# Performance work log

Measured on AMD Instinct MI355X. Metric: run time of the kernel, lower is better.

The kernel has to match this reference:

```python
import jax, jax.numpy as jnp
import numpy as np

BN_EPS = 1e-5

def _conv(x, w, b, pad):
    # x: [B,C,H,W], w: [O,I,kh,kw] -> [B,O,H,W]
    y = jax.lax.conv_general_dilated(x, w, window_strides=(1, 1),
                                     padding=[(pad, pad), (pad, pad)],
                                     dimension_numbers=("NCHW", "OIHW", "NCHW"))
    return y + b[None, :, None, None]

def setup_inputs() -> dict:
    key = jax.random.key(0)
    ks = jax.random.split(key, 5)
    B, Cin, H, W = 2, 256, 80, 80
    Ck, Cv, Cout = 128, 256, 256
    std = 0.02  # matches torch normal_(0, 0.02) init
    return {
        "x": jax.random.normal(ks[0], (B, Cin, H, W), jnp.float32),
        "wk": std * jax.random.normal(ks[1], (Ck, Cin, 1, 1), jnp.float32),
        "bk": jnp.zeros((Ck,), jnp.float32),
        "gamma": jnp.ones((Ck,), jnp.float32),
        "beta": jnp.zeros((Ck,), jnp.float32),
        "rmean": jnp.zeros((Ck,), jnp.float32),
        "rvar": jnp.ones((Ck,), jnp.float32),
        "wv": std * jax.random.normal(ks[2], (Cv, Cin, 3, 3), jnp.float32),
        "bv": jnp.zeros((Cv,), jnp.float32),
        "ww": std * jax.random.normal(ks[3], (Cout, Cv, 1, 1), jnp.float32),
        "bw": jnp.zeros((Cout,), jnp.float32),
    }

def reference(x, wk, bk, gamma, beta, rmean, rvar, wv, bv, ww, bw):
    B, Cin, H, W = x.shape
    Ck, Cv = wk.shape[0], wv.shape[0]
    N = H * W

    # f_key == f_query (shared module): 1x1 conv + BatchNorm (inference stats)
    kq = _conv(x, wk, bk, pad=0)                      # [B,Ck,H,W]
    inv = gamma / jnp.sqrt(rvar + BN_EPS)
    kq = kq * inv[None, :, None, None] + (beta - rmean * inv)[None, :, None, None]
    kq = kq.reshape(B, Ck, N)                          # key layout [B,Ck,N]

    # f_value: 3x3 conv
    value = _conv(x, wv, bv, pad=1).reshape(B, Cv, N)  # [B,Cv,N]

    # sim_map = query^T @ key -> [B,N,N], full softmax over last dim
    sim = jnp.einsum("bcn,bcm->bnm", kq, kq)
    sim = jax.nn.softmax(sim, axis=-1)

    # context = sim @ value^T -> [B,N,Cv] -> [B,Cv,H,W]
    ctx = jnp.einsum("bnm,bcm->bcn", sim, value).reshape(B, Cv, H, W)

    out = _conv(ctx, ww, bw, pad=0) + x                # residual
    return out
```

## Files before the change

### kernel.cpp

```cpp
#include <hip/hip_runtime.h>
#include <math.h>

#define NB   2
#define CIN  256
#define IMH  80
#define IMW  80
#define NPIX (IMH*IMW)
#define CK   128
#define CVC  256
#define COUTC 256
#define BN_EPS 1e-5f
#define HP   82
#define WP   82
#define NMC  (NPIX / 64)
#define LOG2E 1.4426950408889634f
#define M0L  28.853900817779268f

typedef short sx8 __attribute__((ext_vector_type(8)));
typedef short sx4 __attribute__((ext_vector_type(4)));
typedef float f32x4 __attribute__((ext_vector_type(4)));

__device__ __forceinline__ short f2bf(float f) {
    unsigned u = __builtin_bit_cast(unsigned, f);
    u += 0x7fffu + ((u >> 16) & 1u);
    return (short)(u >> 16);
}
__device__ __forceinline__ float bf2f(short s) {
    unsigned u = ((unsigned)(unsigned short)s) << 16;
    return __builtin_bit_cast(float, u);
}
__device__ __forceinline__ int pk_bf16(float a, float b) {
    unsigned ua = __builtin_bit_cast(unsigned, a) + 0x8000u;
    unsigned ub = __builtin_bit_cast(unsigned, b) + 0x8000u;
    return __builtin_amdgcn_perm(ub, ua, 0x07060302);
}

#define WVT_BLKS 256
#define WWB_BLKS 256
#define WKB_BLKS 128
__global__ __launch_bounds__(256) void prep_kernel(
    const float* __restrict__ wv, const float* __restrict__ ww,
    const float* __restrict__ wk, const float* __restrict__ bk,
    const float* __restrict__ gamma, const float* __restrict__ beta,
    const float* __restrict__ rmean, const float* __restrict__ rvar,
    short* __restrict__ wvt, short* __restrict__ wwb,
    short* __restrict__ wkb, float* __restrict__ bias2)
{
    __shared__ short L[9][258];
    const int tid = threadIdx.x;
    const int bx  = blockIdx.x;

    if (bx < WVT_BLKS) {
        const float* src = wv + (size_t)bx * 2304;
        #pragma unroll
        for (int i = 0; i < 9; ++i) {
            int m = i * 256 + tid;
            L[m % 9][m / 9] = f2bf(src[m]);
        }
        __syncthreads();
        #pragma unroll
        for (int j = 0; j < 9; ++j)
            wvt[(size_t)j * (CVC * CIN) + bx * 256 + tid] = L[j][tid];
    } else if (bx < WVT_BLKS + WWB_BLKS) {
        int idx = (bx - WVT_BLKS) * 256 + tid;
        wwb[idx] = f2bf(ww[idx]);
    } else {
        int idx = (bx - WVT_BLKS - WWB_BLKS) * 256 + tid;
        int ck = idx >> 8;
        float inv = gamma[ck] * rsqrtf(rvar[ck] + BN_EPS);
        wkb[idx] = f2bf(wk[idx] * inv);
        if (idx < CK) {
            float invi = gamma[idx] * rsqrtf(rvar[idx] + BN_EPS);
            bias2[idx] = (bk[idx] - rmean[idx]) * invi + beta[idx];
        }
    }
}

__global__ __launch_bounds__(256) void padkq_kernel(
    const float* __restrict__ x, const short* __restrict__ wkb,
    const float* __restrict__ bias2, short* __restrict__ xpad,
    short* __restrict__ kqT)
{
    __shared__ short T[64][258];
    const int tid = threadIdx.x;
    const int n0  = blockIdx.x * 64;
    const int b   = blockIdx.y;
    const float* xb = x + (size_t)b * CIN * NPIX;

    #pragma unroll 4
    for (int i = 0; i < 64; ++i) {
        int e = tid + i * 256;
        int pix = e & 63, c = e >> 6;
        T[pix][c] = f2bf(xb[(size_t)c * NPIX + n0 + pix]);
    }
    __syncthreads();

    #pragma unroll
    for (int i = 0; i < 8; ++i) {
        int e   = tid + i * 256;
        int pix = e >> 5;
        int cp  = (e & 31) * 8;
        int np  = n0 + pix;
        int hp  = np / IMW + 1, wp = np % IMW + 1;
        sx8 v = *(const sx8*)&T[pix][cp];
        *(sx8*)&xpad[(((size_t)b * HP + hp) * WP + wp) * CIN + cp] = v;
    }

    {
        int e = blockIdx.x * 256 + tid;
        if (e < 324 * 32) {
            int p = e >> 5, c8 = (e & 31) * 8;
            int hp, wp;
            if      (p < 82)  { hp = 0;       wp = p;       }
            else if (p < 164) { hp = 81;      wp = p - 82;  }
            else if (p < 244) { hp = p - 163; wp = 0;       }
            else              { hp = p - 243; wp = 81;      }
            sx8 z = {};
            *(sx8*)&xpad[(((size_t)b * HP + hp) * WP + wp) * CIN + c8] = z;
        }
    }

    const int wid  = tid >> 6;
    const int lane = tid & 63;
    const int l15  = lane & 15;
    const int quad = lane >> 4;
    const int ck0  = wid * 32;

    f32x4 acc[2][4];
    #pragma unroll
    for (int at = 0; at < 2; ++at)
        #pragma unroll
        for (int nt = 0; nt < 4; ++nt)
            acc[at][nt] = (f32x4){0.f, 0.f, 0.f, 0.f};

    for (int kc = 0; kc < CIN / 32; ++kc) {
        sx8 af0 = *(const sx8*)&wkb[(size_t)(ck0 + l15) * CIN + kc * 32 + quad * 8];
        sx8 af1 = *(const sx8*)&wkb[(size_t)(ck0 + 16 + l15) * CIN + kc * 32 + quad * 8];
        #pragma unroll
        for (int nt = 0; nt < 4; ++nt) {
            sx8 bf = *(const sx8*)&T[nt * 16 + l15][kc * 32 + quad * 8];
            acc[0][nt] = __builtin_amdgcn_mfma_f32_16x16x32_bf16(af0, bf, acc[0][nt], 0, 0, 0);
            acc[1][nt] = __builtin_amdgcn_mfma_f32_16x16x32_bf16(af1, bf, acc[1][nt], 0, 0, 0);
        }
    }

    __syncthreads();

    #pragma unroll
    for (int at = 0; at < 2; ++at) {
        f32x4 b4 = *(const f32x4*)&bias2[ck0 + at * 16 + quad * 4];
        #pragma unroll
        for (int nt = 0; nt < 4; ++nt)
            #pragma unroll
            for (int r = 0; r < 4; ++r)
                T[nt * 16 + l15][ck0 + at * 16 + quad * 4 + r] = f2bf(acc[at][nt][r] + b4[r]);
    }
    __syncthreads();
    #pragma unroll
    for (int it = 0; it < 4; ++it) {
        int e = tid + it * 256;
        int row = e >> 4, c8 = (e & 15) * 8;
        *(sx8*)&kqT[((size_t)b * NPIX + n0 + row) * CK + c8] = *(const sx8*)&T[row][c8];
    }
}

#define CSTRIDE 36
__global__ __launch_bounds__(512) void conv3_kernel(
    const short* __restrict__ xpad, const short* __restrict__ wvt,
    const float* __restrict__ bv, short* __restrict__ valF)
{
    __shared__ __align__(16) short Xs[2][6 * 18 * CSTRIDE];

    const int tid  = threadIdx.x;
    const int wid  = tid >> 6;
    const int lane = tid & 63;
    const int l15  = lane & 15;
    const int quad = lane >> 4;

    const int rowT = blockIdx.x / 5, colT = blockIdx.x % 5;
    const int h0 = rowT * 4, w0 = colT * 16;
    const int cv0 = blockIdx.y * 128 + wid * 16;
    const int b   = blockIdx.z;

    const short* xb = xpad + (size_t)b * HP * WP * CIN;

    const int rc  = tid >> 2, l4 = tid & 3;
    const int row = rc / 18, col = rc % 18;
    const bool sv = (tid < 432);
    const short* sptr = &xb[(((size_t)(h0 + row)) * WP + (w0 + col)) * CIN + l4 * 8];
    const int sdst = rc * CSTRIDE + l4 * 8;

    f32x4 acc[4];
    #pragma unroll
    for (int r = 0; r < 4; ++r) acc[r] = (f32x4){0.f, 0.f, 0.f, 0.f};

    sx8 v = {};
    if (sv) {
        v = *(const sx8*)&sptr[0];
        *(sx8*)&Xs[0][sdst] = v;
    }
    __syncthreads();

    for (int cc = 0; cc < CIN / 32; ++cc) {
        const int cur = cc & 1;
        if (cc + 1 < CIN / 32 && sv)
            v = *(const sx8*)&sptr[(cc + 1) * 32];

        #pragma unroll
        for (int dw = 0; dw < 3; ++dw) {
            sx8 Bf[6];
            #pragma unroll
            for (int rr = 0; rr < 6; ++rr)
                Bf[rr] = *(const sx8*)&Xs[cur][(rr * 18 + l15 + dw) * CSTRIDE + quad * 8];
            #pragma unroll
            for (int dh = 0; dh < 3; ++dh) {
                int tap = dh * 3 + dw;
                sx8 Af = *(const sx8*)&wvt[((size_t)(tap * 256 + cv0 + l15)) * CIN + cc * 32 + quad * 8];
                #pragma unroll
                for (int r = 0; r < 4; ++r)
                    acc[r] = __builtin_amdgcn_mfma_f32_16x16x32_bf16(Af, Bf[r + dh], acc[r], 0, 0, 0);
            }
        }

        if (cc + 1 < CIN / 32 && sv)
            *(sx8*)&Xs[cur ^ 1][sdst] = v;
        __syncthreads();
    }

    f32x4 bvv = *(const f32x4*)&bv[cv0 + quad * 4];
    const int cvt = cv0 >> 4;
    #pragma unroll
    for (int r = 0; r < 4; ++r) {
        int n  = (h0 + r) * IMW + w0 + l15;
        int mc = n >> 6, s2 = (n >> 5) & 1, qm = (n >> 3) & 3, mi = n & 7;
        size_t base = ((((size_t)(b * NMC + mc) * 16 + cvt) * 2 + s2) * 4 + qm) * 128;
        #pragma unroll
        for (int reg = 0; reg < 4; ++reg)
            valF[base + (quad * 4 + reg) * 8 + mi] = f2bf(acc[r][reg] + bvv[reg]);
    }
}

#define TQ 64
#define TK 64
#define KS_LD 132
#define PS_LD 72

template<int SP>
__global__ __launch_bounds__(512) void attn_kernel(
    const short* __restrict__ kqT, const short* __restrict__ valF,
    short* __restrict__ opart, float* __restrict__ lpart)
{
    constexpr int NCc  = NPIX / SP / 64;
    constexpr int SPSH = (SP == 4) ? 3 : 2;

    __shared__ __align__(16) short Ks[TK][KS_LD];
    __shared__ __align__(16) short Pb[TQ][PS_LD];
    __shared__ float lqs[2][64];

    const int tid  = threadIdx.x;
    const int wid  = tid >> 6;
    const int lane = tid & 63;
    const int l15  = lane & 15;
    const int quad = lane >> 4;
    const int qw   = wid & 3;
    const int mh   = wid >> 2;

    const int blk = blockIdx.x;
    const int b   = blk & 1;
    const int sp  = (blk >> 1) & (SP - 1);
    const int n0  = (blk >> SPSH) * TQ;
    const int mb  = sp * (NPIX / SP);

    const short* kqb = kqT + (size_t)b * NPIX * CK;
    const short* vbase = valF + ((size_t)(b * NMC + sp * NCc) * 16 + wid * 2) * 1024
                              + (size_t)lane * 8;

    const int srow = tid >> 4;
    const int sc8  = (tid & 15) * 8;

    sx8 qf[4];
    #pragma unroll
    for (int s = 0; s < 4; ++s)
        qf[s] = *(const sx8*)&kqb[(size_t)(n0 + qw * 16 + l15) * CK + s * 32 + quad * 8];

    sx8 kreg[2];
    #pragma unroll
    for (int p = 0; p < 2; ++p)
        kreg[p] = *(const sx8*)&kqb[(size_t)(mb + srow + p * 32) * CK + sc8];
    #pragma unroll
    for (int p = 0; p < 2; ++p)
        *(sx8*)&Ks[srow + p * 32][sc8] = kreg[p];

    sx8 vreg[4];
    #pragma unroll
    for (int ct = 0; ct < 2; ++ct)
        #pragma unroll
        for (int s2 = 0; s2 < 2; ++s2)
            vreg[ct * 2 + s2] = *(const sx8*)&vbase[ct * 1024 + s2 * 512];

    float lq = 0.f;
    f32x4 acc[4][2];
    #pragma unroll
    for (int qt = 0; qt < 4; ++qt)
        #pragma unroll
        for (int ct = 0; ct < 2; ++ct)
            acc[qt][ct] = (f32x4){0.f, 0.f, 0.f, 0.f};

    __syncthreads();

    for (int i = 0; i < NCc; ++i) {
        if (i + 1 < NCc) {
            #pragma unroll
            for (int p = 0; p < 2; ++p)
                kreg[p] = *(const sx8*)&kqb[(size_t)(mb + (i + 1) * TK + srow + p * 32) * CK + sc8];
        }

        f32x4 st[2];
        #pragma unroll
        for (int t2 = 0; t2 < 2; ++t2) st[t2] = (f32x4){0.f, 0.f, 0.f, 0.f};
        #pragma unroll
        for (int s = 0; s < 4; ++s) {
            sx8 af[2];
            #pragma unroll
            for (int t2 = 0; t2 < 2; ++t2)
                af[t2] = *(const sx8*)&Ks[mh * 32 + t2 * 16 + l15][s * 32 + quad * 8];
            #pragma unroll
            for (int t2 = 0; t2 < 2; ++t2)
                st[t2] = __builtin_amdgcn_mfma_f32_16x16x32_bf16(af[t2], qf[s], st[t2], 0, 0, 0);
        }

        __syncthreads();

        #pragma unroll
        for (int t2 = 0; t2 < 2; ++t2)
            #pragma unroll
            for (int r = 0; r < 4; ++r)
                st[t2][r] = exp2f(fmaf(st[t2][r], LOG2E, -M0L));

        if (i + 1 < NCc) {
            #pragma unroll
            for (int p = 0; p < 2; ++p)
                *(sx8*)&Ks[srow + p * 32][sc8] = kreg[p];
        }

        #pragma unroll
        for (int t2 = 0; t2 < 2; ++t2) {
            int2 pw;
            pw.x = pk_bf16(st[t2][0], st[t2][1]);
            pw.y = pk_bf16(st[t2][2], st[t2][3]);
            *(int2*)&Pb[qw * 16 + l15][mh * 32 + t2 * 16 + quad * 4] = pw;
        }

        lq += (st[0][0] + st[0][1]) + (st[0][2] + st[0][3])
            + (st[1][0] + st[1][1]) + (st[1][2] + st[1][3]);

        __syncthreads();

        #pragma unroll
        for (int s2 = 0; s2 < 2; ++s2) {
            sx8 pa[4];
            #pragma unroll
            for (int qt = 0; qt < 4; ++qt)
                pa[qt] = *(const sx8*)&Pb[qt * 16 + l15][s2 * 32 + quad * 8];
            #pragma unroll
            for (int ct = 0; ct < 2; ++ct) {
                #pragma unroll
                for (int qt = 0; qt < 4; ++qt)
                    acc[qt][ct] = __builtin_amdgcn_mfma_f32_16x16x32_bf16(pa[qt], vreg[ct * 2 + s2], acc[qt][ct], 0, 0, 0);
            }
        }

        if (i + 1 < NCc) {
            #pragma unroll
            for (int ct = 0; ct < 2; ++ct)
                #pragma unroll
                for (int s2 = 0; s2 < 2; ++s2)
                    vreg[ct * 2 + s2] = *(const sx8*)&vbase[(size_t)(i + 1) * 16384 + ct * 1024 + s2 * 512];
        }
    }

    lq += __shfl_xor(lq, 16);
    lq += __shfl_xor(lq, 32);
    if (quad == 0)
        lqs[mh][qw * 16 + l15] = lq;

    size_t obase = (size_t)(sp * NB + b) * NPIX + n0;
    #pragma unroll
    for (int qt = 0; qt < 4; ++qt)
        #pragma unroll
        for (int ct = 0; ct < 2; ++ct) {
            int cv = wid * 32 + ct * 16 + l15;
            #pragma unroll
            for (int r = 0; r < 4; ++r)
                opart[(obase + qt * 16 + quad * 4 + r) * CVC + cv] = f2bf(acc[qt][ct][r]);
        }

    __syncthreads();
    if (tid < 64)
        lpart[obase + tid] = lqs[0][tid] + lqs[1][tid];
}

#define BS_LD 40
template<int SP>
__global__ __launch_bounds__(512) void out_kernel(
    const short* __restrict__ opart, const float* __restrict__ lpart,
    const short* __restrict__ wwb, const float* __restrict__ bw,
    const float* __restrict__ x, float* __restrict__ out)
{
    __shared__ __align__(16) short Bs[2][64][BS_LD];
    __shared__ float rinvs[64];

    const int tid  = threadIdx.x;
    const int wid  = tid >> 6;
    const int lane = tid & 63;
    const int l15  = lane & 15;
    const int quad = lane >> 4;

    const int n0  = blockIdx.x * 64;
    const int co0 = blockIdx.y * 128 + wid * 16;
    const int b   = blockIdx.z;

    if (tid < 64) {
        int n = n0 + tid;
        float ls = 0.f;
        #pragma unroll
        for (int s = 0; s < SP; ++s)
            ls += lpart[(size_t)(s * NB + b) * NPIX + n];
        rinvs[tid] = 1.f / ls;
    }

    const int srow = tid >> 2;
    const int sc8  = (tid & 3) * 8;
    const short* op0 = opart + ((size_t)b * NPIX + n0 + srow) * CVC + sc8;
    constexpr size_t SSTR = (size_t)NB * NPIX * CVC;
    const bool sv = (tid < 256);

    __syncthreads();

    if (sv) {
        float ri = rinvs[srow];
        float sacc[8] = {0.f, 0.f, 0.f, 0.f, 0.f, 0.f, 0.f, 0.f};
        #pragma unroll
        for (int s = 0; s < SP; ++s) {
            sx8 a = *(const sx8*)&op0[s * SSTR];
            #pragma unroll
            for (int j = 0; j < 8; ++j)
                sacc[j] += bf2f(a[j]);
        }
        sx8 o;
        #pragma unroll
        for (int j = 0; j < 8; ++j)
            o[j] = f2bf(sacc[j] * ri);
        *(sx8*)&Bs[0][srow][sc8] = o;
    }
    __syncthreads();

    f32x4 acc[4];
    #pragma unroll
    for (int nt = 0; nt < 4; ++nt) acc[nt] = (f32x4){0.f, 0.f, 0.f, 0.f};

    for (int cc = 0; cc < CVC / 32; ++cc) {
        const int cur = cc & 1;
        const bool st = (cc + 1 < CVC / 32) && sv;

        sx8 a[SP];
        if (st) {
            #pragma unroll
            for (int s = 0; s < SP; ++s)
                a[s] = *(const sx8*)&op0[s * SSTR + (cc + 1) * 32];
        }

        sx8 af = *(const sx8*)&wwb[(size_t)(co0 + l15) * CVC + cc * 32 + quad * 8];
        #pragma unroll
        for (int nt = 0; nt < 4; ++nt) {
            sx8 bf = *(const sx8*)&Bs[cur][nt * 16 + l15][quad * 8];
            acc[nt] = __builtin_amdgcn_mfma_f32_16x16x32_bf16(af, bf, acc[nt], 0, 0, 0);
        }

        if (st) {
            float ri = rinvs[srow];
            float sacc[8] = {0.f, 0.f, 0.f, 0.f, 0.f, 0.f, 0.f, 0.f};
            #pragma unroll
            for (int s = 0; s < SP; ++s)
                #pragma unroll
                for (int j = 0; j < 8; ++j)
                    sacc[j] += bf2f(a[s][j]);
            sx8 o;
            #pragma unroll
            for (int j = 0; j < 8; ++j)
                o[j] = f2bf(sacc[j] * ri);
            *(sx8*)&Bs[cur ^ 1][srow][sc8] = o;
        }
        __syncthreads();
    }

    f32x4 bv4 = *(const f32x4*)&bw[co0 + quad * 4];
    #pragma unroll
    for (int nt = 0; nt < 4; ++nt) {
        #pragma unroll
        for (int r = 0; r < 4; ++r) {
            int co = co0 + quad * 4 + r;
            int n  = n0 + nt * 16 + l15;
            size_t gi = ((size_t)b * COUTC + co) * NPIX + n;
            out[gi] = acc[nt][r] + bv4[r] + x[gi];
        }
    }
}

extern "C" void kernel_launch(void* const* d_in, const int* in_sizes, int n_in,
                              void* d_out, int out_size, void* d_ws, size_t ws_size,
                              hipStream_t stream)
{
    const float* x     = (const float*)d_in[0];
    const float* wk    = (const float*)d_in[1];
    const float* bk    = (const float*)d_in[2];
    const float* gamma = (const float*)d_in[3];
    const float* beta  = (const float*)d_in[4];
    const float* rmean = (const float*)d_in[5];
    const float* rvar  = (const float*)d_in[6];
    const float* wv    = (const float*)d_in[7];
    const float* bv    = (const float*)d_in[8];
    const float* ww    = (const float*)d_in[9];
    const float* bw    = (const float*)d_in[10];
    float* out = (float*)d_out;

    const size_t perSplit = (size_t)NB * NPIX * CVC;
    const size_t persistShorts = (size_t)COUTC * CVC + (size_t)CK * CIN
                               + (size_t)NB * NPIX * CK + (size_t)NB * NPIX * CVC;
    const size_t need4 = 2ull * (4ull * perSplit + persistShorts)
                       + 4ull * (CK + 4ull * NB * NPIX);
    const int SPL = (ws_size >= need4) ? 4 : 2;

    short* opart = (short*)d_ws;
    short* xpad  = opart;
    short* wvt   = xpad + (size_t)NB * HP * WP * CIN;
    short* wwb   = opart + (size_t)SPL * perSplit;
    short* wkb   = wwb  + (size_t)COUTC * CVC;
    short* kqT   = wkb  + (size_t)CK * CIN;
    short* valF  = kqT  + (size_t)NB * NPIX * CK;
    float* bias2 = (float*)(valF + perSplit);
    float* lpart = bias2 + CK;

    prep_kernel  <<<WVT_BLKS + WWB_BLKS + WKB_BLKS, 256, 0, stream>>>(
        wv, ww, wk, bk, gamma, beta, rmean, rvar, wvt, wwb, wkb, bias2);
    padkq_kernel <<<dim3(NPIX/64, NB),          256, 0, stream>>>(x, wkb, bias2, xpad, kqT);
    conv3_kernel <<<dim3(100, CVC/128,     NB), 512, 0, stream>>>(xpad, wvt, bv, valF);

    if (SPL == 4) {
        attn_kernel<4> <<<NB * 4 * (NPIX / TQ), 512, 0, stream>>>(kqT, valF, opart, lpart);
        out_kernel<4>  <<<dim3(100, COUTC/128, NB), 512, 0, stream>>>(opart, lpart, wwb, bw, x, out);
    } else {
        attn_kernel<2> <<<NB * 2 * (NPIX / TQ), 512, 0, stream>>>(kqT, valF, opart, lpart);
        out_kernel<2>  <<<dim3(100, COUTC/128, NB), 512, 0, stream>>>(opart, lpart, wwb, bw, x, out);
    }
}
```

Measured before the change: 231.6 us.

## Cover all output channels per out_kernel block and fix attention split at 2

Each out_kernel block now computes all 256 output channels: every wave handles 32 channels with two MFMA accumulator sets. This halves the grid, and the split-K reduction and normalisation of the attention partials is done once per pixel tile instead of twice. The attention split count is also hardcoded to 2 instead of choosing 4 when the workspace allows. The trade-offs are fewer blocks (200), which lowers parallelism for the output GEMM, and less parallelism in the attention kernel when 4 splits were previously used.

```diff
diff --git a/kernel.cpp b/kernel.cpp
--- a/kernel.cpp
+++ b/kernel.cpp
@@ -417,8 +417,8 @@
     const int quad = lane >> 4;
 
     const int n0  = blockIdx.x * 64;
-    const int co0 = blockIdx.y * 128 + wid * 16;
-    const int b   = blockIdx.z;
+    const int co0 = wid * 32;
+    const int b   = blockIdx.y;
 
     if (tid < 64) {
         int n = n0 + tid;
@@ -455,9 +455,12 @@
     }
     __syncthreads();
 
-    f32x4 acc[4];
-    #pragma unroll
-    for (int nt = 0; nt < 4; ++nt) acc[nt] = (f32x4){0.f, 0.f, 0.f, 0.f};
+    f32x4 acc[4][2];
+    #pragma unroll
+    for (int nt = 0; nt < 4; ++nt)
+        #pragma unroll
+        for (int ct = 0; ct < 2; ++ct)
+            acc[nt][ct] = (f32x4){0.f, 0.f, 0.f, 0.f};
 
     for (int cc = 0; cc < CVC / 32; ++cc) {
         const int cur = cc & 1;
@@ -470,11 +473,16 @@
                 a[s] = *(const sx8*)&op0[s * SSTR + (cc + 1) * 32];
         }
 
-        sx8 af = *(const sx8*)&wwb[(size_t)(co0 + l15) * CVC + cc * 32 + quad * 8];
+        sx8 af[2];
+        #pragma unroll
+        for (int ct = 0; ct < 2; ++ct)
+            af[ct] = *(const sx8*)&wwb[(size_t)(co0 + ct * 16 + l15) * CVC + cc * 32 + quad * 8];
         #pragma unroll
         for (int nt = 0; nt < 4; ++nt) {
             sx8 bf = *(const sx8*)&Bs[cur][nt * 16 + l15][quad * 8];
-            acc[nt] = __builtin_amdgcn_mfma_f32_16x16x32_bf16(af, bf, acc[nt], 0, 0, 0);
+            #pragma unroll
+            for (int ct = 0; ct < 2; ++ct)
+                acc[nt][ct] = __builtin_amdgcn_mfma_f32_16x16x32_bf16(af[ct], bf, acc[nt][ct], 0, 0, 0);
         }
 
         if (st) {
@@ -494,15 +502,18 @@
         __syncthreads();
     }
 
-    f32x4 bv4 = *(const f32x4*)&bw[co0 + quad * 4];
-    #pragma unroll
-    for (int nt = 0; nt < 4; ++nt) {
-        #pragma unroll
-        for (int r = 0; r < 4; ++r) {
-            int co = co0 + quad * 4 + r;
-            int n  = n0 + nt * 16 + l15;
-            size_t gi = ((size_t)b * COUTC + co) * NPIX + n;
-            out[gi] = acc[nt][r] + bv4[r] + x[gi];
+    #pragma unroll
+    for (int ct = 0; ct < 2; ++ct) {
+        f32x4 bv4 = *(const f32x4*)&bw[co0 + ct * 16 + quad * 4];
+        #pragma unroll
+        for (int nt = 0; nt < 4; ++nt) {
+            #pragma unroll
+            for (int r = 0; r < 4; ++r) {
+                int co = co0 + ct * 16 + quad * 4 + r;
+                int n  = n0 + nt * 16 + l15;
+                size_t gi = ((size_t)b * COUTC + co) * NPIX + n;
+                out[gi] = acc[nt][ct][r] + bv4[r] + x[gi];
+            }
         }
     }
 }
@@ -524,12 +535,8 @@
     const float* bw    = (const float*)d_in[10];
     float* out = (float*)d_out;
 
+    constexpr int SPL = 2;
     const size_t perSplit = (size_t)NB * NPIX * CVC;
-    const size_t persistShorts = (size_t)COUTC * CVC + (size_t)CK * CIN
-                               + (size_t)NB * NPIX * CK + (size_t)NB * NPIX * CVC;
-    const size_t need4 = 2ull * (4ull * perSplit + persistShorts)
-                       + 4ull * (CK + 4ull * NB * NPIX);
-    const int SPL = (ws_size >= need4) ? 4 : 2;
 
     short* opart = (short*)d_ws;
     short* xpad  = opart;
@@ -545,12 +552,6 @@
         wv, ww, wk, bk, gamma, beta, rmean, rvar, wvt, wwb, wkb, bias2);
     padkq_kernel <<<dim3(NPIX/64, NB),          256, 0, stream>>>(x, wkb, bias2, xpad, kqT);
     conv3_kernel <<<dim3(100, CVC/128,     NB), 512, 0, stream>>>(xpad, wvt, bv, valF);
-
-    if (SPL == 4) {
-        attn_kernel<4> <<<NB * 4 * (NPIX / TQ), 512, 0, stream>>>(kqT, valF, opart, lpart);
-        out_kernel<4>  <<<dim3(100, COUTC/128, NB), 512, 0, stream>>>(opart, lpart, wwb, bw, x, out);
-    } else {
-        attn_kernel<2> <<<NB * 2 * (NPIX / TQ), 512, 0, stream>>>(kqT, valF, opart, lpart);
-        out_kernel<2>  <<<dim3(100, COUTC/128, NB), 512, 0, stream>>>(opart, lpart, wwb, bw, x, out);
-    }
-}
+    attn_kernel<SPL> <<<NB * SPL * (NPIX / TQ), 512, 0, stream>>>(kqT, valF, opart, lpart);
+    out_kernel<SPL>  <<<dim3(100, NB),          512, 0, stream>>>(opart, lpart, wwb, bw, x, out);
+}
```

After: 223.8 us, median of 2. -3.4%, faster.
